# Performance work log

Measured on AMD Instinct MI355X. Metric: run time of the kernel, lower is better.

The kernel has to match this reference:

```python
import jax, jax.numpy as jnp
import numpy as np

NHEAD = 16
DHEAD = 128  # dim_embed // nhead
ROPE_BASE = 10000.0


def rmsnorm(x, g):
    eps = jnp.finfo(x.dtype).eps  # torch nn.RMSNorm default eps=None -> dtype eps
    return x * jax.lax.rsqrt(jnp.mean(x * x, axis=-1, keepdims=True) + eps) * g


def rope(x):
    # torchtune-style interleaved RoPE. x: [B,S,H,D]
    B, S, H, D = x.shape
    freqs = 1.0 / (ROPE_BASE ** (jnp.arange(0, D, 2, dtype=jnp.float32) / D))  # [D/2]
    ang = jnp.arange(S, dtype=jnp.float32)[:, None] * freqs[None, :]           # [S,D/2]
    cos = jnp.cos(ang)[None, :, None, :]
    sin = jnp.sin(ang)[None, :, None, :]
    x1, x2 = x[..., 0::2], x[..., 1::2]
    return jnp.stack([x1 * cos - x2 * sin, x1 * sin + x2 * cos], axis=-1).reshape(B, S, H, D)


def setup_inputs() -> dict:
    key = jax.random.key(0)
    B, S, E, C = 4, 2048, 2048, 512
    ks = jax.random.split(key, 9)
    std = 0.02
    h = jax.random.normal(ks[0], (B, S, E), jnp.float32)
    w_d_kv = jax.random.normal(ks[1], (C, E), jnp.float32) * std
    w_u_k = jax.random.normal(ks[2], (E, C), jnp.float32) * std
    w_u_v = jax.random.normal(ks[3], (E, C), jnp.float32) * std
    w_d_q = jax.random.normal(ks[4], (C, E), jnp.float32) * std
    w_u_q = jax.random.normal(ks[5], (E, C), jnp.float32) * std
    w_kr = jax.random.normal(ks[6], (E, E), jnp.float32) * std
    w_qr = jax.random.normal(ks[7], (E, C), jnp.float32) * std
    w_o = jax.random.normal(ks[8], (E, E), jnp.float32) * std
    g1 = jnp.ones((C,), jnp.float32)
    g2 = jnp.ones((C,), jnp.float32)
    g3 = jnp.ones((E,), jnp.float32)
    return {"h": h, "w_d_kv": w_d_kv, "w_u_k": w_u_k, "w_u_v": w_u_v,
            "w_d_q": w_d_q, "w_u_q": w_u_q, "w_kr": w_kr, "w_qr": w_qr,
            "w_o": w_o, "g1": g1, "g2": g2, "g3": g3}


def reference(h, w_d_kv, w_u_k, w_u_v, w_d_q, w_u_q, w_kr, w_qr, w_o, g1, g2, g3):
    # Eval (inference) path of MLA with absorbed weights; no kv/kr cache.
    B, S, E = h.shape
    cq = rmsnorm(h @ w_d_q.T, g1)          # [B,S,C]
    ckv = rmsnorm(h @ w_d_kv.T, g2)        # [B,S,C]
    qr = rope((cq @ w_qr.T).reshape(B, S, NHEAD, DHEAD)).reshape(B, S, E)
    kr = rope((h @ w_kr.T).reshape(B, S, NHEAD, DHEAD)).reshape(B, S, E)
    # absorbed_w_q = (w_d_q.T @ w_u_q.T) @ w_u_k : [E,C]
    absorbed_w_q = (w_d_q.T @ w_u_q.T) @ w_u_k
    # absorbed_w_o = w_u_v.T @ w_o.T : [C,E]
    absorbed_w_o = w_u_v.T @ w_o.T
    aq = h @ absorbed_w_q                  # [B,S,C]  (note: raw h, as in source)
    scores = jnp.einsum('bsc,btc->bst', aq, ckv) + jnp.einsum('bse,bte->bst', qr, kr)
    attn = jax.nn.softmax(scores / np.float32(np.sqrt(NHEAD + DHEAD)), axis=-1)
    o = jnp.einsum('bst,btc->bsc', attn, ckv)
    u = rmsnorm(o @ absorbed_w_o, g3)      # [B,S,E]
    return (u, ckv, kr)
```

## Files before the change

kernel.cpp:

```cpp
#include <hip/hip_runtime.h>
#include <stdint.h>

typedef __attribute__((ext_vector_type(8))) short bf16x8;
typedef __attribute__((ext_vector_type(8))) unsigned short u16x8;
typedef __attribute__((ext_vector_type(4))) float floatx4;

__device__ __forceinline__ uint16_t f2bf(float f) {
  union { float f; uint32_t u; } v; v.f = f;
  uint32_t r = v.u + 0x7fffu + ((v.u >> 16) & 1u);
  return (uint16_t)(r >> 16);
}
__device__ __forceinline__ float bf2f(uint16_t b) {
  union { uint32_t u; float f; } v; v.u = ((uint32_t)b) << 16;
  return v.f;
}
__device__ __forceinline__ float ld_as_float(float v) { return v; }
__device__ __forceinline__ float ld_as_float(uint16_t v) { return bf2f(v); }

__device__ __forceinline__ void mfma16(floatx4& d, bf16x8 a, bf16x8 b) {
  asm("v_mfma_f32_16x16x32_bf16 %0, %1, %2, %0" : "+v"(d) : "v"(a), "v"(b));
}

#define FENCE() asm volatile("" ::: "memory")
#define SCHED() __builtin_amdgcn_sched_barrier(0)
#define SBAR()                                  \
  do {                                          \
    FENCE();                                    \
    __builtin_amdgcn_sched_barrier(0);          \
    __builtin_amdgcn_s_barrier();               \
    __builtin_amdgcn_sched_barrier(0);          \
    FENCE();                                    \
  } while (0)

template<int MODE>
__global__ void __launch_bounds__(512, 1) gemm256v3(
    const uint16_t* __restrict__ A, const uint16_t* __restrict__ B,
    void* __restrict__ C0v, void* __restrict__ C1v, void* __restrict__ C2v,
    int K, int lda, int ldb, int ldc,
    long sA, long sB, long sC)
{
  __shared__ __attribute__((aligned(16))) char lds[131072];
  const int tid = threadIdx.x;
  const int w = tid >> 6, l = tid & 63;
  const int wm = w >> 2, wn = w & 3;

  const int gx = gridDim.x;
  const int nwg = gx * gridDim.y;
  int id = blockIdx.y * gx + blockIdx.x;
  if ((nwg & 7) == 0) id = (id & 7) * (nwg >> 3) + (id >> 3);
  const long bm = (long)(id % gx) * 256;
  const long bn = (long)(id / gx) * 256;
  A += (long)blockIdx.z * sA;
  B += (long)blockIdx.z * sB;

  const int scol = (((l & 3) ^ ((l >> 3) & 3)) << 3);
  const uint16_t* gA = A + (bm + w * 16 + (l >> 2)) * (long)lda + scol;
  const uint16_t* gB = B + (bn + w * 16 + (l >> 2)) * (long)ldb + scol;
  const int ldsw = w * 1024;

#define STG_A3(slot, k0, r)                                                    \
  __builtin_amdgcn_global_load_lds(gA + (k0) + (long)(r) * 128 * lda,          \
      (uint16_t*)(lds + (slot) * 32768 + (r) * 8192 + ldsw), 16, 0, 0)
#define STG_B3(slot, k0, r)                                                    \
  __builtin_amdgcn_global_load_lds(gB + (k0) + (long)(r) * 128 * ldb,          \
      (uint16_t*)(lds + (slot) * 32768 + 16384 + (r) * 8192 + ldsw), 16, 0, 0)

  const int lr = l & 15;
  const int chunkx = (((l >> 4) ^ ((lr >> 1) & 3)) << 4);
  const int aoff = (wm * 128 + lr) * 64 + chunkx;
  const int boff = 16384 + (wn * 64 + lr) * 64 + chunkx;

  floatx4 acc[8][4];
#pragma unroll
  for (int i = 0; i < 8; i++)
#pragma unroll
    for (int j = 0; j < 4; j++) acc[i][j] = (floatx4){0.f, 0.f, 0.f, 0.f};

  const int nt = K >> 5;
#pragma unroll
  for (int tt = 0; tt < 3; tt++) {
    STG_A3(tt, tt * 32, 0); STG_A3(tt, tt * 32, 1);
    STG_B3(tt, tt * 32, 0); STG_B3(tt, tt * 32, 1);
  }

  for (int t = 0; t < nt; t++) {
    const char* Ls = lds + (t & 3) * 32768;
    if (t + 2 < nt) asm volatile("s_waitcnt vmcnt(8)" ::: "memory");
    else            asm volatile("s_waitcnt vmcnt(0)" ::: "memory");
    SBAR();

    bf16x8 Bf[4], Af0[4], Af1[4];
#pragma unroll
    for (int j = 0; j < 4; j++) Bf[j] = *(const bf16x8*)(Ls + boff + j * 1024);
#pragma unroll
    for (int i = 0; i < 4; i++) Af0[i] = *(const bf16x8*)(Ls + aoff + i * 1024);
    SCHED();

    const long pk0 = (long)(t + 3) << 5;
    const int pslot = (t + 3) & 3;
    const bool pf = (t + 3 < nt);
    if (pf) { STG_A3(pslot, pk0, 0); STG_A3(pslot, pk0, 1); }

#pragma unroll
    for (int i = 0; i < 4; i++) Af1[i] = *(const bf16x8*)(Ls + aoff + (4 + i) * 1024);
    SCHED();

    asm volatile("s_waitcnt lgkmcnt(4)" ::: "memory");
    SCHED();
    __builtin_amdgcn_s_setprio(1);
#pragma unroll
    for (int i = 0; i < 4; i++)
#pragma unroll
      for (int j = 0; j < 4; j++) mfma16(acc[i][j], Af0[i], Bf[j]);
    __builtin_amdgcn_s_setprio(0);
    SCHED();

    if (pf) { STG_B3(pslot, pk0, 0); STG_B3(pslot, pk0, 1); }

    asm volatile("s_waitcnt lgkmcnt(0)" ::: "memory");
    SCHED();
    __builtin_amdgcn_s_setprio(1);
#pragma unroll
    for (int i = 0; i < 4; i++)
#pragma unroll
      for (int j = 0; j < 4; j++) mfma16(acc[4 + i][j], Af1[i], Bf[j]);
    __builtin_amdgcn_s_setprio(0);
    SCHED();
  }
#undef STG_A3
#undef STG_B3

  const long crow = bm + wm * 128 + ((l >> 4) * 4);
  const long ccol = bn + wn * 64 + (l & 15);
  if constexpr (MODE == 0) {
    float* C = (float*)C0v + (long)blockIdx.z * sC;
#pragma unroll
    for (int i = 0; i < 8; i++)
#pragma unroll
      for (int r = 0; r < 4; r++) {
        long row = crow + i * 16 + r;
#pragma unroll
        for (int j = 0; j < 4; j++) C[row * (long)ldc + ccol + j * 16] = acc[i][j][r];
      }
  } else if constexpr (MODE == 1) {
    uint16_t* C = (uint16_t*)C0v + (long)blockIdx.z * sC;
#pragma unroll
    for (int i = 0; i < 8; i++)
#pragma unroll
      for (int r = 0; r < 4; r++) {
        long row = crow + i * 16 + r;
#pragma unroll
        for (int j = 0; j < 4; j++) C[row * (long)ldc + ccol + j * 16] = f2bf(acc[i][j][r]);
      }
  } else if constexpr (MODE == 3) {
    const float s = 1.0f / 12.0f;
    uint16_t* C = (uint16_t*)C0v + (long)blockIdx.z * sC;
#pragma unroll
    for (int i = 0; i < 8; i++)
#pragma unroll
      for (int r = 0; r < 4; r++) {
        long row = crow + i * 16 + r;
#pragma unroll
        for (int j = 0; j < 4; j++) C[row * (long)ldc + ccol + j * 16] = f2bf(acc[i][j][r] * s);
      }
  } else {
    if (bn < 512) {
      uint16_t* C = (uint16_t*)C0v;
#pragma unroll
      for (int i = 0; i < 8; i++)
#pragma unroll
        for (int r = 0; r < 4; r++) {
          long row = crow + i * 16 + r;
#pragma unroll
          for (int j = 0; j < 4; j++) C[row * 512 + ccol + j * 16] = f2bf(acc[i][j][r]);
        }
    } else if (bn < 1024) {
      float* C = (float*)C1v;
      const long cc = ccol - 512;
#pragma unroll
      for (int i = 0; i < 8; i++)
#pragma unroll
        for (int r = 0; r < 4; r++) {
          long row = crow + i * 16 + r;
#pragma unroll
          for (int j = 0; j < 4; j++) C[row * 512 + cc + j * 16] = acc[i][j][r];
        }
    } else {
      uint16_t* C = (uint16_t*)C2v;
      const long cc = ccol - 1024;
#pragma unroll
      for (int i = 0; i < 8; i++)
#pragma unroll
        for (int r = 0; r < 4; r++) {
          long row = crow + i * 16 + r;
#pragma unroll
          for (int j = 0; j < 4; j++) C[row * 2560 + cc + j * 16] = f2bf(acc[i][j][r]);
        }
    }
  }
}

template<int OUTB>
__global__ void __launch_bounds__(512, 2) gemm256(
    const uint16_t* __restrict__ A, const uint16_t* __restrict__ B,
    void* __restrict__ Cv, int K, int lda, int ldb, int ldc,
    long sA, long sB, long sC)
{
  __shared__ __attribute__((aligned(16))) char lds[147456];
  const int tid = threadIdx.x;
  const int w = tid >> 6, l = tid & 63;
  const int wm = w >> 1, wn = w & 1;

  const int gx = gridDim.x;
  const int nwg = gx * gridDim.y;
  int id = blockIdx.y * gx + blockIdx.x;
  if ((nwg & 7) == 0) id = (id & 7) * (nwg >> 3) + (id >> 3);
  const long bm = (long)(id % gx) * 256;
  const long bn = (long)(id / gx) * 128;
  A += (long)blockIdx.z * sA;
  B += (long)blockIdx.z * sB;

  const int sr = l >> 3;
  const int sc = l & 7;
  const int scol = ((sc ^ sr) << 3);
  const uint16_t* gA = A + (bm + w * 8 + sr) * (long)lda + scol;
  const uint16_t* gB = B + (bn + w * 8 + sr) * (long)ldb + scol;
  const int ldsw = w * 1024;

#define STAGE_A(bufi, k0, r)                                                     \
  __builtin_amdgcn_global_load_lds(gA + (k0) + (long)(r) * 64 * lda,             \
      (uint16_t*)(lds + (bufi) * 49152 + (r) * 8192 + ldsw), 16, 0, 0)
#define STAGE_B(bufi, k0, r)                                                     \
  __builtin_amdgcn_global_load_lds(gB + (k0) + (long)(r) * 64 * ldb,             \
      (uint16_t*)(lds + (bufi) * 49152 + 32768 + (r) * 8192 + ldsw), 16, 0, 0)

  const int lr = l & 15;
  const int kk = (l >> 4) << 4;
  const int msk = (l & 7) << 4;
  const int ko0 = kk ^ msk;
  const int ko1 = (64 + kk) ^ msk;
  const int arow = (wm * 64 + lr) * 128;
  const int brow = (wn * 64 + lr) * 128;

  floatx4 acc[4][4];
#pragma unroll
  for (int i = 0; i < 4; i++)
#pragma unroll
    for (int j = 0; j < 4; j++) acc[i][j] = (floatx4){0.f, 0.f, 0.f, 0.f};

  const int nt = K >> 6;
#pragma unroll
  for (int r = 0; r < 4; r++) STAGE_A(0, 0, r);
#pragma unroll
  for (int r = 0; r < 2; r++) STAGE_B(0, 0, r);
#pragma unroll
  for (int r = 0; r < 4; r++) STAGE_A(1, 64, r);
#pragma unroll
  for (int r = 0; r < 2; r++) STAGE_B(1, 64, r);
  asm volatile("s_waitcnt vmcnt(6)" ::: "memory");
  SBAR();

  bf16x8 af0[4], bf0[4], af1[4], bf1[4];
  {
    const char* LA = lds + arow;
    const char* LB = lds + 32768 + brow;
#pragma unroll
    for (int i = 0; i < 4; i++) af0[i] = *(const bf16x8*)(LA + i * 2048 + ko0);
#pragma unroll
    for (int j = 0; j < 4; j++) bf0[j] = *(const bf16x8*)(LB + j * 2048 + ko0);
  }

  for (int t = 0; t < nt; t++) {
    const int buf = t % 3;
    const int pbuf = (t + 2) % 3;
    const long pk0 = (long)(t + 2) << 6;
    const char* LA = lds + buf * 49152 + arow;
    const char* LB = lds + buf * 49152 + 32768 + brow;
    const bool pf = (t + 2 < nt);

    if (pf) { STAGE_A(pbuf, pk0, 0); STAGE_A(pbuf, pk0, 1); STAGE_B(pbuf, pk0, 0); }
#pragma unroll
    for (int i = 0; i < 4; i++) af1[i] = *(const bf16x8*)(LA + i * 2048 + ko1);
#pragma unroll
    for (int j = 0; j < 4; j++) bf1[j] = *(const bf16x8*)(LB + j * 2048 + ko1);
    SCHED();
    __builtin_amdgcn_s_setprio(1);
#pragma unroll
    for (int i = 0; i < 4; i++)
#pragma unroll
      for (int j = 0; j < 4; j++) mfma16(acc[i][j], af0[i], bf0[j]);
    __builtin_amdgcn_s_setprio(0);
    SCHED();

    if (pf) { STAGE_A(pbuf, pk0, 2); STAGE_A(pbuf, pk0, 3); STAGE_B(pbuf, pk0, 1); }
    if (t < nt - 2) asm volatile("s_waitcnt vmcnt(6) lgkmcnt(0)" ::: "memory");
    else            asm volatile("s_waitcnt vmcnt(0) lgkmcnt(0)" ::: "memory");
    SBAR();
    if (t < nt - 1) {
      const char* LAn = lds + ((t + 1) % 3) * 49152 + arow;
      const char* LBn = lds + ((t + 1) % 3) * 49152 + 32768 + brow;
#pragma unroll
      for (int i = 0; i < 4; i++) af0[i] = *(const bf16x8*)(LAn + i * 2048 + ko0);
#pragma unroll
      for (int j = 0; j < 4; j++) bf0[j] = *(const bf16x8*)(LBn + j * 2048 + ko0);
    }
    SCHED();
    __builtin_amdgcn_s_setprio(1);
#pragma unroll
    for (int i = 0; i < 4; i++)
#pragma unroll
      for (int j = 0; j < 4; j++) mfma16(acc[i][j], af1[i], bf1[j]);
    __builtin_amdgcn_s_setprio(0);
    SCHED();
  }
#undef STAGE_A
#undef STAGE_B

  const long crow = bm + wm * 64 + ((l >> 4) * 4);
  const long ccol = bn + wn * 64 + (l & 15);
  if constexpr (OUTB == 0) {
    float* C = (float*)Cv + (long)blockIdx.z * sC;
#pragma unroll
    for (int i = 0; i < 4; i++)
#pragma unroll
      for (int r = 0; r < 4; r++) {
        long row = crow + i * 16 + r;
#pragma unroll
        for (int j = 0; j < 4; j++) C[row * (long)ldc + ccol + j * 16] = acc[i][j][r];
      }
  } else {
    uint16_t* C = (uint16_t*)Cv + (long)blockIdx.z * sC;
#pragma unroll
    for (int i = 0; i < 4; i++)
#pragma unroll
      for (int r = 0; r < 4; r++) {
        long row = crow + i * 16 + r;
#pragma unroll
        for (int j = 0; j < 4; j++) C[row * (long)ldc + ccol + j * 16] = f2bf(acc[i][j][r]);
      }
  }
}

template<int OUTB>
__global__ void __launch_bounds__(256) gemm_bt(
    const uint16_t* __restrict__ A, const uint16_t* __restrict__ B,
    void* __restrict__ Cv, int K, int lda, int ldb, int ldc,
    long sA, long sB, long sC)
{
  __shared__ alignas(16) uint16_t As[4096];
  __shared__ alignas(16) uint16_t Bs[4096];
  const int tid = threadIdx.x;
  const int w = tid >> 6, l = tid & 63;
  const int wr = w >> 1, wc = w & 1;
  const long bm = (long)blockIdx.x * 128, bn = (long)blockIdx.y * 128;
  A += (long)blockIdx.z * sA;
  B += (long)blockIdx.z * sB;

  const uint16_t* ga0 = A + (bm + w * 16 + (l >> 2)) * (long)lda + (l & 3) * 8;
  const uint16_t* ga1 = ga0 + 64L * lda;
  const uint16_t* gb0 = B + (bn + w * 16 + (l >> 2)) * (long)ldb + (l & 3) * 8;
  const uint16_t* gb1 = gb0 + 64L * ldb;
  uint16_t* la0 = &As[w * 512];
  uint16_t* la1 = &As[2048 + w * 512];
  uint16_t* lb0 = &Bs[w * 512];
  uint16_t* lb1 = &Bs[2048 + w * 512];

  floatx4 acc[4][4];
#pragma unroll
  for (int i = 0; i < 4; i++)
#pragma unroll
    for (int j = 0; j < 4; j++) acc[i][j] = (floatx4){0.f, 0.f, 0.f, 0.f};

  const int rA = (wr * 64 + (l & 15)) * 32 + (l >> 4) * 8;
  const int rB = (wc * 64 + (l & 15)) * 32 + (l >> 4) * 8;

  for (int k0 = 0; k0 < K; k0 += 32) {
    __builtin_amdgcn_global_load_lds(ga0, la0, 16, 0, 0);
    __builtin_amdgcn_global_load_lds(ga1, la1, 16, 0, 0);
    __builtin_amdgcn_global_load_lds(gb0, lb0, 16, 0, 0);
    __builtin_amdgcn_global_load_lds(gb1, lb1, 16, 0, 0);
    ga0 += 32; ga1 += 32; gb0 += 32; gb1 += 32;
    __syncthreads();
    bf16x8 af[4], bfr[4];
#pragma unroll
    for (int i = 0; i < 4; i++) af[i] = *(const bf16x8*)&As[rA + i * 512];
#pragma unroll
    for (int j = 0; j < 4; j++) bfr[j] = *(const bf16x8*)&Bs[rB + j * 512];
#pragma unroll
    for (int i = 0; i < 4; i++)
#pragma unroll
      for (int j = 0; j < 4; j++) mfma16(acc[i][j], af[i], bfr[j]);
    __syncthreads();
  }

  const long crow = bm + wr * 64 + ((l >> 4) * 4);
  const long ccol = bn + wc * 64 + (l & 15);
  if constexpr (OUTB == 0) {
    float* C = (float*)Cv + (long)blockIdx.z * sC;
#pragma unroll
    for (int i = 0; i < 4; i++)
#pragma unroll
      for (int r = 0; r < 4; r++) {
        long row = crow + i * 16 + r;
#pragma unroll
        for (int j = 0; j < 4; j++) C[row * (long)ldc + ccol + j * 16] = acc[i][j][r];
      }
  } else {
    uint16_t* C = (uint16_t*)Cv + (long)blockIdx.z * sC;
#pragma unroll
    for (int i = 0; i < 4; i++)
#pragma unroll
      for (int r = 0; r < 4; r++) {
        long row = crow + i * 16 + r;
#pragma unroll
        for (int j = 0; j < 4; j++) C[row * (long)ldc + ccol + j * 16] = f2bf(acc[i][j][r]);
      }
  }
}

__global__ void __launch_bounds__(256) cvt_k(const float* __restrict__ in,
                                             uint16_t* __restrict__ out, long n) {
  long i = ((long)blockIdx.x * 256 + threadIdx.x) * 4;
  if (i >= n) return;
  float4 v = *(const float4*)(in + i);
  ushort4 o; o.x = f2bf(v.x); o.y = f2bf(v.y); o.z = f2bf(v.z); o.w = f2bf(v.w);
  *(ushort4*)(out + i) = o;
}

__global__ void __launch_bounds__(256) prep_small(
    const float* __restrict__ wdq, const float* __restrict__ wdkv,
    const float* __restrict__ wqr, const float* __restrict__ wkr,
    const float* __restrict__ wo,
    uint16_t* __restrict__ wdq_b, uint16_t* __restrict__ wdkv_b,
    uint16_t* __restrict__ wqr_b, uint16_t* __restrict__ wkr_b,
    uint16_t* __restrict__ wo_b, float2* __restrict__ rtab)
{
  const int b = blockIdx.x;
  if (b < 11264) {
    const float* src; uint16_t* dst; long off;
    if (b < 1024)      { src = wdq;  dst = wdq_b;  off = b; }
    else if (b < 2048) { src = wdkv; dst = wdkv_b; off = b - 1024; }
    else if (b < 3072) { src = wqr;  dst = wqr_b;  off = b - 2048; }
    else if (b < 7168) { src = wkr;  dst = wkr_b;  off = b - 3072; }
    else               { src = wo;   dst = wo_b;   off = b - 7168; }
    long i = (off * 256 + threadIdx.x) * 4;
    float4 v = *(const float4*)(src + i);
    ushort4 o; o.x = f2bf(v.x); o.y = f2bf(v.y); o.z = f2bf(v.z); o.w = f2bf(v.w);
    *(ushort4*)(dst + i) = o;
  } else {
    int idx = (b - 11264) * 256 + threadIdx.x;
    int s = idx >> 6, fi = idx & 63;
    float f = powf(10000.0f, -(float)fi * (1.0f / 64.0f));
    float ang = (float)s * f;
    rtab[idx] = make_float2(cosf(ang), sinf(ang));
  }
}

template<typename TIN>
__global__ void __launch_bounds__(256) transpose_to_bf16(
    const TIN* __restrict__ in, uint16_t* __restrict__ out,
    int ld_in, int ld_out, long sIn, long sOut)
{
  __shared__ float tile[32][33];
  in += (long)blockIdx.z * sIn;
  out += (long)blockIdx.z * sOut;
  const int rb = blockIdx.y * 32, cb = blockIdx.x * 32;
#pragma unroll
  for (int i = 0; i < 32; i += 8)
    tile[threadIdx.y + i][threadIdx.x] =
        ld_as_float(in[(long)(rb + threadIdx.y + i) * ld_in + cb + threadIdx.x]);
  __syncthreads();
#pragma unroll
  for (int i = 0; i < 32; i += 8)
    out[(long)(cb + threadIdx.y + i) * ld_out + rb + threadIdx.x] =
        f2bf(tile[threadIdx.x][threadIdx.y + i]);
}

template<int PT, typename TIN>
__global__ void __launch_bounds__(256) rmsnorm_k(
    const TIN* __restrict__ in, const float* __restrict__ g,
    float* __restrict__ out_f, uint16_t* __restrict__ out_b, int ld_b)
{
  constexpr int DIM = PT * 256;
  __shared__ float sm[9];
  const TIN* x = in + (long)blockIdx.x * DIM;
  const int base = threadIdx.x * PT;
  float v[PT];
  if constexpr (sizeof(TIN) == 2) {
    if constexpr (PT >= 8) {
#pragma unroll
      for (int i = 0; i < PT; i += 8) {
        u16x8 t = *(const u16x8*)&x[base + i];
#pragma unroll
        for (int q = 0; q < 8; q++) v[i + q] = bf2f(t[q]);
      }
    } else {
#pragma unroll
      for (int i = 0; i < PT; i += 2) {
        ushort2 t = *(const ushort2*)&x[base + i];
        v[i] = bf2f(t.x); v[i + 1] = bf2f(t.y);
      }
    }
  } else if constexpr (PT == 2) {
    float2 t = *(const float2*)&x[base]; v[0] = t.x; v[1] = t.y;
  } else {
#pragma unroll
    for (int i = 0; i < PT; i += 4) {
      float4 t = *(const float4*)&x[base + i];
      v[i] = t.x; v[i + 1] = t.y; v[i + 2] = t.z; v[i + 3] = t.w;
    }
  }
  float ss = 0.f;
#pragma unroll
  for (int i = 0; i < PT; i++) ss += v[i] * v[i];
#pragma unroll
  for (int o = 32; o; o >>= 1) ss += __shfl_down(ss, o);
  if ((threadIdx.x & 63) == 0) sm[threadIdx.x >> 6] = ss;
  __syncthreads();
  if (threadIdx.x == 0)
    sm[8] = rsqrtf((sm[0] + sm[1] + sm[2] + sm[3]) * (1.0f / DIM) + 1.1920929e-7f);
  __syncthreads();
  const float sc = sm[8];
#pragma unroll
  for (int i = 0; i < PT; i++) {
    float y = v[i] * sc * g[base + i];
    if (out_f) out_f[(long)blockIdx.x * DIM + base + i] = y;
    if (out_b) out_b[(long)blockIdx.x * ld_b + base + i] = f2bf(y);
  }
}

template<bool WF32>
__global__ void __launch_bounds__(256) rope_k(
    const uint16_t* __restrict__ in, uint16_t* __restrict__ outb,
    float* __restrict__ outf, const float2* __restrict__ tab)
{
  long idx = (long)blockIdx.x * 256 + threadIdx.x;
  int r = (int)(idx >> 10);
  int pp = (int)idx & 1023;
  int s = r & 2047;
  int fi = pp & 63;
  ushort2 xv = *(const ushort2*)(in + ((long)r << 11) + 2 * pp);
  float x0 = bf2f(xv.x), x1 = bf2f(xv.y);
  float2 cs = tab[(s << 6) + fi];
  float y0 = x0 * cs.x - x1 * cs.y;
  float y1 = x0 * cs.y + x1 * cs.x;
  ushort2 ov; ov.x = f2bf(y0); ov.y = f2bf(y1);
  *(ushort2*)(outb + (long)r * 2560 + 512 + 2 * pp) = ov;
  if (WF32) *(float2*)(outf + ((long)r << 11) + 2 * pp) = make_float2(y0, y1);
}

__global__ void __launch_bounds__(256) softmax_k(const uint16_t* __restrict__ sc,
                                                 uint16_t* __restrict__ attn) {
  __shared__ float sm[9];
  const uint16_t* x = sc + ((long)blockIdx.x << 11);
  const int base = threadIdx.x * 8;
  float v[8];
  u16x8 t = *(const u16x8*)&x[base];
#pragma unroll
  for (int i = 0; i < 8; i++) v[i] = bf2f(t[i]);
  float m = -1e30f;
#pragma unroll
  for (int i = 0; i < 8; i++) m = fmaxf(m, v[i]);
#pragma unroll
  for (int o = 32; o; o >>= 1) m = fmaxf(m, __shfl_down(m, o));
  if ((threadIdx.x & 63) == 0) sm[threadIdx.x >> 6] = m;
  __syncthreads();
  if (threadIdx.x == 0)
    sm[8] = fmaxf(fmaxf(sm[0], sm[1]), fmaxf(sm[2], sm[3]));
  __syncthreads();
  m = sm[8];
  __syncthreads();
  float ss = 0.f;
#pragma unroll
  for (int i = 0; i < 8; i++) { v[i] = __expf(v[i] - m); ss += v[i]; }
#pragma unroll
  for (int o = 32; o; o >>= 1) ss += __shfl_down(ss, o);
  if ((threadIdx.x & 63) == 0) sm[threadIdx.x >> 6] = ss;
  __syncthreads();
  if (threadIdx.x == 0) sm[8] = 1.0f / (sm[0] + sm[1] + sm[2] + sm[3]);
  __syncthreads();
  const float r = sm[8];
  ushort4 o1, o2;
  o1.x = f2bf(v[0] * r); o1.y = f2bf(v[1] * r); o1.z = f2bf(v[2] * r); o1.w = f2bf(v[3] * r);
  o2.x = f2bf(v[4] * r); o2.y = f2bf(v[5] * r); o2.z = f2bf(v[6] * r); o2.w = f2bf(v[7] * r);
  uint16_t* dst = attn + ((long)blockIdx.x << 11) + base;
  *(ushort4*)dst = o1;
  *(ushort4*)(dst + 4) = o2;
}

extern "C" void kernel_launch(void* const* d_in, const int* in_sizes, int n_in,
                              void* d_out, int out_size, void* d_ws, size_t ws_size,
                              hipStream_t stream) {
  (void)in_sizes; (void)n_in; (void)out_size; (void)ws_size;
  const float* h    = (const float*)d_in[0];
  const float* wdkv = (const float*)d_in[1];
  const float* wuk  = (const float*)d_in[2];
  const float* wuv  = (const float*)d_in[3];
  const float* wdq  = (const float*)d_in[4];
  const float* wuq  = (const float*)d_in[5];
  const float* wkr  = (const float*)d_in[6];
  const float* wqr  = (const float*)d_in[7];
  const float* wo   = (const float*)d_in[8];
  const float* g1   = (const float*)d_in[9];
  const float* g2   = (const float*)d_in[10];
  const float* g3   = (const float*)d_in[11];

  float* u_out   = (float*)d_out;
  float* ckv_out = u_out + 16777216L;
  float* kr_out  = ckv_out + 4194304L;

  char* p = (char*)d_ws;
  auto alloc = [&](size_t bytes) -> void* {
    void* q = (void*)p; p += (bytes + 255) & ~(size_t)255; return q;
  };
  uint16_t* hb     = (uint16_t*)alloc(16777216ULL * 2);
  uint16_t* wcat   = (uint16_t*)alloc(3145728ULL * 2);
  uint16_t* wqr_b  = (uint16_t*)alloc(1048576ULL * 2);
  uint16_t* wkr_b  = (uint16_t*)alloc(4194304ULL * 2);
  uint16_t* wo_b   = (uint16_t*)alloc(4194304ULL * 2);
  uint16_t* wukT   = (uint16_t*)alloc(1048576ULL * 2);
  uint16_t* wuqT   = (uint16_t*)alloc(1048576ULL * 2);
  uint16_t* wuvT   = (uint16_t*)alloc(1048576ULL * 2);
  uint16_t* wdqT   = (uint16_t*)alloc(1048576ULL * 2);
  uint16_t* T1t    = (uint16_t*)alloc(262144ULL * 2);
  uint16_t* awoT   = (uint16_t*)alloc(1048576ULL * 2);
  uint16_t* cqpre  = (uint16_t*)alloc(4194304ULL * 2);
  uint16_t* cq_b   = (uint16_t*)alloc(4194304ULL * 2);
  uint16_t* catq   = (uint16_t*)alloc(20971520ULL * 2);
  uint16_t* catk   = (uint16_t*)alloc(20971520ULL * 2);
  uint16_t* ckvT   = (uint16_t*)alloc(4194304ULL * 2);
  uint16_t* o_b    = (uint16_t*)alloc(4194304ULL * 2);
  float2*   rtab   = (float2*)alloc(131072ULL * 8);
  float*    tmpS2  = (float*)alloc(4194304ULL * 4);
  float*    tmpB   = (float*)alloc(16777216ULL * 4);
  uint16_t* tmpBb  = (uint16_t*)tmpB;
  uint16_t* attn   = catq;

  uint16_t* wdq_b  = wcat;
  uint16_t* wdkv_b = wcat + 1048576;
  uint16_t* Bqt    = wcat + 2097152;

  const dim3 b256(256);
  const dim3 b512(512);
  const dim3 tb(32, 8);

  cvt_k<<<dim3(16384), b256, 0, stream>>>(h, hb, 16777216L);
  prep_small<<<dim3(11776), b256, 0, stream>>>(
      wdq, wdkv, wqr, wkr, wo, wdq_b, wdkv_b, wqr_b, wkr_b, wo_b, rtab);
  transpose_to_bf16<float><<<dim3(16, 64, 1), tb, 0, stream>>>(wuk, wukT, 512, 2048, 0, 0);
  transpose_to_bf16<float><<<dim3(16, 64, 1), tb, 0, stream>>>(wuq, wuqT, 512, 2048, 0, 0);
  transpose_to_bf16<float><<<dim3(16, 64, 1), tb, 0, stream>>>(wuv, wuvT, 512, 2048, 0, 0);
  transpose_to_bf16<float><<<dim3(64, 16, 1), tb, 0, stream>>>(wdq, wdqT, 2048, 512, 0, 0);

  gemm_bt<1><<<dim3(4, 4, 1), b256, 0, stream>>>(wukT, wuqT, T1t, 2048, 2048, 2048, 512, 0, 0, 0);
  gemm_bt<1><<<dim3(4, 16, 1), b256, 0, stream>>>(T1t, wdqT, Bqt, 512, 512, 512, 2048, 0, 0, 0);
  gemm_bt<1><<<dim3(16, 4, 1), b256, 0, stream>>>(wo_b, wuvT, awoT, 2048, 2048, 2048, 512, 0, 0, 0);

  gemm256v3<2><<<dim3(32, 6, 1), b512, 0, stream>>>(
      hb, wcat, cqpre, tmpS2, catq, 2048, 2048, 2048, 0, 0, 0, 0);
  rmsnorm_k<2, uint16_t><<<dim3(8192), b256, 0, stream>>>(cqpre, g1, nullptr, cq_b, 512);
  gemm256v3<1><<<dim3(32, 8, 1), b512, 0, stream>>>(
      cq_b, wqr_b, tmpBb, nullptr, nullptr, 512, 512, 512, 2048, 0, 0, 0);
  rope_k<false><<<dim3(32768), b256, 0, stream>>>(tmpBb, catq, nullptr, rtab);
  rmsnorm_k<2, float><<<dim3(8192), b256, 0, stream>>>(tmpS2, g2, ckv_out, catk, 2560);
  transpose_to_bf16<uint16_t><<<dim3(16, 64, 4), tb, 0, stream>>>(
      catk, ckvT, 2560, 2048, 2048L * 2560, 512L * 2048);
  gemm256v3<1><<<dim3(32, 8, 1), b512, 0, stream>>>(
      hb, wkr_b, tmpBb, nullptr, nullptr, 2048, 2048, 2048, 2048, 0, 0, 0);
  rope_k<true><<<dim3(32768), b256, 0, stream>>>(tmpBb, catk, kr_out, rtab);
  gemm256v3<3><<<dim3(8, 8, 4), b512, 0, stream>>>(
      catq, catk, tmpBb, nullptr, nullptr, 2560, 2560, 2560, 2048,
      5242880L, 5242880L, 4194304L);
  softmax_k<<<dim3(8192), b256, 0, stream>>>(tmpBb, attn);
  gemm256<1><<<dim3(8, 4, 4), b512, 0, stream>>>(
      attn, ckvT, o_b, 2048, 2048, 2048, 512, 4194304L, 1048576L, 1048576L);
  gemm256v3<1><<<dim3(32, 8, 1), b512, 0, stream>>>(
      o_b, awoT, tmpBb, nullptr, nullptr, 512, 512, 512, 2048, 0, 0, 0);
  rmsnorm_k<8, uint16_t><<<dim3(8192), b256, 0, stream>>>(tmpBb, g3, u_out, nullptr, 0);
}
```

Measured before the change: 551.5 us.

## Replace 256x256 GEMMs with 256x128 two-block-per-CU kernel and split-K weight absorption

Replaces the 512-thread 256x256 GEMM kernels with a 256-thread, 256x128-tile kernel. It uses a 3-slot LDS ring and launch bounds that allow two workgroups per CU, and it doubles grid sizes to match. The aim is better CU fill and latency hiding on the mid-sized projection and attention GEMMs. The K=2048 weight-absorption GEMMs are now split four ways along K, writing fp32 partials that a new reduceK kernel sums and converts to bf16. This exposes more parallelism for those small-output products, at the cost of extra launches and partial-buffer traffic.

```diff
diff --git a/kernel.cpp b/kernel.cpp
--- a/kernel.cpp
+++ b/kernel.cpp
@@ -33,180 +33,13 @@
   } while (0)
 
 template<int MODE>
-__global__ void __launch_bounds__(512, 1) gemm256v3(
+__global__ void __launch_bounds__(256, 2) gemm128(
     const uint16_t* __restrict__ A, const uint16_t* __restrict__ B,
     void* __restrict__ C0v, void* __restrict__ C1v, void* __restrict__ C2v,
     int K, int lda, int ldb, int ldc,
     long sA, long sB, long sC)
 {
-  __shared__ __attribute__((aligned(16))) char lds[131072];
-  const int tid = threadIdx.x;
-  const int w = tid >> 6, l = tid & 63;
-  const int wm = w >> 2, wn = w & 3;
-
-  const int gx = gridDim.x;
-  const int nwg = gx * gridDim.y;
-  int id = blockIdx.y * gx + blockIdx.x;
-  if ((nwg & 7) == 0) id = (id & 7) * (nwg >> 3) + (id >> 3);
-  const long bm = (long)(id % gx) * 256;
-  const long bn = (long)(id / gx) * 256;
-  A += (long)blockIdx.z * sA;
-  B += (long)blockIdx.z * sB;
-
-  const int scol = (((l & 3) ^ ((l >> 3) & 3)) << 3);
-  const uint16_t* gA = A + (bm + w * 16 + (l >> 2)) * (long)lda + scol;
-  const uint16_t* gB = B + (bn + w * 16 + (l >> 2)) * (long)ldb + scol;
-  const int ldsw = w * 1024;
-
-#define STG_A3(slot, k0, r)                                                    \
-  __builtin_amdgcn_global_load_lds(gA + (k0) + (long)(r) * 128 * lda,          \
-      (uint16_t*)(lds + (slot) * 32768 + (r) * 8192 + ldsw), 16, 0, 0)
-#define STG_B3(slot, k0, r)                                                    \
-  __builtin_amdgcn_global_load_lds(gB + (k0) + (long)(r) * 128 * ldb,          \
-      (uint16_t*)(lds + (slot) * 32768 + 16384 + (r) * 8192 + ldsw), 16, 0, 0)
-
-  const int lr = l & 15;
-  const int chunkx = (((l >> 4) ^ ((lr >> 1) & 3)) << 4);
-  const int aoff = (wm * 128 + lr) * 64 + chunkx;
-  const int boff = 16384 + (wn * 64 + lr) * 64 + chunkx;
-
-  floatx4 acc[8][4];
-#pragma unroll
-  for (int i = 0; i < 8; i++)
-#pragma unroll
-    for (int j = 0; j < 4; j++) acc[i][j] = (floatx4){0.f, 0.f, 0.f, 0.f};
-
-  const int nt = K >> 5;
-#pragma unroll
-  for (int tt = 0; tt < 3; tt++) {
-    STG_A3(tt, tt * 32, 0); STG_A3(tt, tt * 32, 1);
-    STG_B3(tt, tt * 32, 0); STG_B3(tt, tt * 32, 1);
-  }
-
-  for (int t = 0; t < nt; t++) {
-    const char* Ls = lds + (t & 3) * 32768;
-    if (t + 2 < nt) asm volatile("s_waitcnt vmcnt(8)" ::: "memory");
-    else            asm volatile("s_waitcnt vmcnt(0)" ::: "memory");
-    SBAR();
-
-    bf16x8 Bf[4], Af0[4], Af1[4];
-#pragma unroll
-    for (int j = 0; j < 4; j++) Bf[j] = *(const bf16x8*)(Ls + boff + j * 1024);
-#pragma unroll
-    for (int i = 0; i < 4; i++) Af0[i] = *(const bf16x8*)(Ls + aoff + i * 1024);
-    SCHED();
-
-    const long pk0 = (long)(t + 3) << 5;
-    const int pslot = (t + 3) & 3;
-    const bool pf = (t + 3 < nt);
-    if (pf) { STG_A3(pslot, pk0, 0); STG_A3(pslot, pk0, 1); }
-
-#pragma unroll
-    for (int i = 0; i < 4; i++) Af1[i] = *(const bf16x8*)(Ls + aoff + (4 + i) * 1024);
-    SCHED();
-
-    asm volatile("s_waitcnt lgkmcnt(4)" ::: "memory");
-    SCHED();
-    __builtin_amdgcn_s_setprio(1);
-#pragma unroll
-    for (int i = 0; i < 4; i++)
-#pragma unroll
-      for (int j = 0; j < 4; j++) mfma16(acc[i][j], Af0[i], Bf[j]);
-    __builtin_amdgcn_s_setprio(0);
-    SCHED();
-
-    if (pf) { STG_B3(pslot, pk0, 0); STG_B3(pslot, pk0, 1); }
-
-    asm volatile("s_waitcnt lgkmcnt(0)" ::: "memory");
-    SCHED();
-    __builtin_amdgcn_s_setprio(1);
-#pragma unroll
-    for (int i = 0; i < 4; i++)
-#pragma unroll
-      for (int j = 0; j < 4; j++) mfma16(acc[4 + i][j], Af1[i], Bf[j]);
-    __builtin_amdgcn_s_setprio(0);
-    SCHED();
-  }
-#undef STG_A3
-#undef STG_B3
-
-  const long crow = bm + wm * 128 + ((l >> 4) * 4);
-  const long ccol = bn + wn * 64 + (l & 15);
-  if constexpr (MODE == 0) {
-    float* C = (float*)C0v + (long)blockIdx.z * sC;
-#pragma unroll
-    for (int i = 0; i < 8; i++)
-#pragma unroll
-      for (int r = 0; r < 4; r++) {
-        long row = crow + i * 16 + r;
-#pragma unroll
-        for (int j = 0; j < 4; j++) C[row * (long)ldc + ccol + j * 16] = acc[i][j][r];
-      }
-  } else if constexpr (MODE == 1) {
-    uint16_t* C = (uint16_t*)C0v + (long)blockIdx.z * sC;
-#pragma unroll
-    for (int i = 0; i < 8; i++)
-#pragma unroll
-      for (int r = 0; r < 4; r++) {
-        long row = crow + i * 16 + r;
-#pragma unroll
-        for (int j = 0; j < 4; j++) C[row * (long)ldc + ccol + j * 16] = f2bf(acc[i][j][r]);
-      }
-  } else if constexpr (MODE == 3) {
-    const float s = 1.0f / 12.0f;
-    uint16_t* C = (uint16_t*)C0v + (long)blockIdx.z * sC;
-#pragma unroll
-    for (int i = 0; i < 8; i++)
-#pragma unroll
-      for (int r = 0; r < 4; r++) {
-        long row = crow + i * 16 + r;
-#pragma unroll
-        for (int j = 0; j < 4; j++) C[row * (long)ldc + ccol + j * 16] = f2bf(acc[i][j][r] * s);
-      }
-  } else {
-    if (bn < 512) {
-      uint16_t* C = (uint16_t*)C0v;
-#pragma unroll
-      for (int i = 0; i < 8; i++)
-#pragma unroll
-        for (int r = 0; r < 4; r++) {
-          long row = crow + i * 16 + r;
-#pragma unroll
-          for (int j = 0; j < 4; j++) C[row * 512 + ccol + j * 16] = f2bf(acc[i][j][r]);
-        }
-    } else if (bn < 1024) {
-      float* C = (float*)C1v;
-      const long cc = ccol - 512;
-#pragma unroll
-      for (int i = 0; i < 8; i++)
-#pragma unroll
-        for (int r = 0; r < 4; r++) {
-          long row = crow + i * 16 + r;
-#pragma unroll
-          for (int j = 0; j < 4; j++) C[row * 512 + cc + j * 16] = acc[i][j][r];
-        }
-    } else {
-      uint16_t* C = (uint16_t*)C2v;
-      const long cc = ccol - 1024;
-#pragma unroll
-      for (int i = 0; i < 8; i++)
-#pragma unroll
-        for (int r = 0; r < 4; r++) {
-          long row = crow + i * 16 + r;
-#pragma unroll
-          for (int j = 0; j < 4; j++) C[row * 2560 + cc + j * 16] = f2bf(acc[i][j][r]);
-        }
-    }
-  }
-}
-
-template<int OUTB>
-__global__ void __launch_bounds__(512, 2) gemm256(
-    const uint16_t* __restrict__ A, const uint16_t* __restrict__ B,
-    void* __restrict__ Cv, int K, int lda, int ldb, int ldc,
-    long sA, long sB, long sC)
-{
-  __shared__ __attribute__((aligned(16))) char lds[147456];
+  __shared__ __attribute__((aligned(16))) char lds[73728];
   const int tid = threadIdx.x;
   const int w = tid >> 6, l = tid & 63;
   const int wm = w >> 1, wn = w & 1;
@@ -220,124 +53,152 @@
   A += (long)blockIdx.z * sA;
   B += (long)blockIdx.z * sB;
 
-  const int sr = l >> 3;
-  const int sc = l & 7;
-  const int scol = ((sc ^ sr) << 3);
-  const uint16_t* gA = A + (bm + w * 8 + sr) * (long)lda + scol;
-  const uint16_t* gB = B + (bn + w * 8 + sr) * (long)ldb + scol;
+  const int scol = (((l & 3) ^ ((l >> 3) & 3)) << 3);
+  const uint16_t* gA = A + (bm + w * 16 + (l >> 2)) * (long)lda + scol;
+  const uint16_t* gB = B + (bn + w * 16 + (l >> 2)) * (long)ldb + scol;
   const int ldsw = w * 1024;
 
-#define STAGE_A(bufi, k0, r)                                                     \
-  __builtin_amdgcn_global_load_lds(gA + (k0) + (long)(r) * 64 * lda,             \
-      (uint16_t*)(lds + (bufi) * 49152 + (r) * 8192 + ldsw), 16, 0, 0)
-#define STAGE_B(bufi, k0, r)                                                     \
-  __builtin_amdgcn_global_load_lds(gB + (k0) + (long)(r) * 64 * ldb,             \
-      (uint16_t*)(lds + (bufi) * 49152 + 32768 + (r) * 8192 + ldsw), 16, 0, 0)
+#define STG_A4(slot, k0, r)                                                    \
+  __builtin_amdgcn_global_load_lds(gA + (k0) + (long)(r) * 64 * lda,           \
+      (uint16_t*)(lds + (slot) * 24576 + (r) * 4096 + ldsw), 16, 0, 0)
+#define STG_B4(slot, k0, r)                                                    \
+  __builtin_amdgcn_global_load_lds(gB + (k0) + (long)(r) * 64 * ldb,           \
+      (uint16_t*)(lds + (slot) * 24576 + 16384 + (r) * 4096 + ldsw), 16, 0, 0)
 
   const int lr = l & 15;
-  const int kk = (l >> 4) << 4;
-  const int msk = (l & 7) << 4;
-  const int ko0 = kk ^ msk;
-  const int ko1 = (64 + kk) ^ msk;
-  const int arow = (wm * 64 + lr) * 128;
-  const int brow = (wn * 64 + lr) * 128;
-
-  floatx4 acc[4][4];
-#pragma unroll
-  for (int i = 0; i < 4; i++)
+  const int chunkx = (((l >> 4) ^ ((lr >> 1) & 3)) << 4);
+  const int aoff = (wm * 128 + lr) * 64 + chunkx;
+  const int boff = 16384 + (wn * 64 + lr) * 64 + chunkx;
+
+  floatx4 acc[8][4];
+#pragma unroll
+  for (int i = 0; i < 8; i++)
 #pragma unroll
     for (int j = 0; j < 4; j++) acc[i][j] = (floatx4){0.f, 0.f, 0.f, 0.f};
 
-  const int nt = K >> 6;
-#pragma unroll
-  for (int r = 0; r < 4; r++) STAGE_A(0, 0, r);
-#pragma unroll
-  for (int r = 0; r < 2; r++) STAGE_B(0, 0, r);
-#pragma unroll
-  for (int r = 0; r < 4; r++) STAGE_A(1, 64, r);
-#pragma unroll
-  for (int r = 0; r < 2; r++) STAGE_B(1, 64, r);
-  asm volatile("s_waitcnt vmcnt(6)" ::: "memory");
-  SBAR();
-
-  bf16x8 af0[4], bf0[4], af1[4], bf1[4];
-  {
-    const char* LA = lds + arow;
-    const char* LB = lds + 32768 + brow;
-#pragma unroll
-    for (int i = 0; i < 4; i++) af0[i] = *(const bf16x8*)(LA + i * 2048 + ko0);
-#pragma unroll
-    for (int j = 0; j < 4; j++) bf0[j] = *(const bf16x8*)(LB + j * 2048 + ko0);
+  const int nt = K >> 5;
+#pragma unroll
+  for (int tt = 0; tt < 2; tt++) {
+    STG_A4(tt, tt * 32, 0); STG_A4(tt, tt * 32, 1);
+    STG_A4(tt, tt * 32, 2); STG_A4(tt, tt * 32, 3);
+    STG_B4(tt, tt * 32, 0); STG_B4(tt, tt * 32, 1);
   }
 
   for (int t = 0; t < nt; t++) {
-    const int buf = t % 3;
-    const int pbuf = (t + 2) % 3;
-    const long pk0 = (long)(t + 2) << 6;
-    const char* LA = lds + buf * 49152 + arow;
-    const char* LB = lds + buf * 49152 + 32768 + brow;
+    const char* Ls = lds + (t % 3) * 24576;
+    if (t < nt - 1) asm volatile("s_waitcnt vmcnt(6)" ::: "memory");
+    else            asm volatile("s_waitcnt vmcnt(0)" ::: "memory");
+    SBAR();
+
+    bf16x8 Bf[4], Af0[4], Af1[4];
+#pragma unroll
+    for (int j = 0; j < 4; j++) Bf[j] = *(const bf16x8*)(Ls + boff + j * 1024);
+#pragma unroll
+    for (int i = 0; i < 4; i++) Af0[i] = *(const bf16x8*)(Ls + aoff + i * 1024);
+    SCHED();
+
+    const long pk0 = (long)(t + 2) << 5;
+    const int pslot = (t + 2) % 3;
     const bool pf = (t + 2 < nt);
-
-    if (pf) { STAGE_A(pbuf, pk0, 0); STAGE_A(pbuf, pk0, 1); STAGE_B(pbuf, pk0, 0); }
-#pragma unroll
-    for (int i = 0; i < 4; i++) af1[i] = *(const bf16x8*)(LA + i * 2048 + ko1);
-#pragma unroll
-    for (int j = 0; j < 4; j++) bf1[j] = *(const bf16x8*)(LB + j * 2048 + ko1);
+    if (pf) { STG_A4(pslot, pk0, 0); STG_A4(pslot, pk0, 1); }
+
+#pragma unroll
+    for (int i = 0; i < 4; i++) Af1[i] = *(const bf16x8*)(Ls + aoff + (4 + i) * 1024);
+    SCHED();
+    if (pf) { STG_A4(pslot, pk0, 2); STG_A4(pslot, pk0, 3); }
+
+    asm volatile("s_waitcnt lgkmcnt(4)" ::: "memory");
     SCHED();
     __builtin_amdgcn_s_setprio(1);
 #pragma unroll
     for (int i = 0; i < 4; i++)
 #pragma unroll
-      for (int j = 0; j < 4; j++) mfma16(acc[i][j], af0[i], bf0[j]);
+      for (int j = 0; j < 4; j++) mfma16(acc[i][j], Af0[i], Bf[j]);
     __builtin_amdgcn_s_setprio(0);
     SCHED();
 
-    if (pf) { STAGE_A(pbuf, pk0, 2); STAGE_A(pbuf, pk0, 3); STAGE_B(pbuf, pk0, 1); }
-    if (t < nt - 2) asm volatile("s_waitcnt vmcnt(6) lgkmcnt(0)" ::: "memory");
-    else            asm volatile("s_waitcnt vmcnt(0) lgkmcnt(0)" ::: "memory");
-    SBAR();
-    if (t < nt - 1) {
-      const char* LAn = lds + ((t + 1) % 3) * 49152 + arow;
-      const char* LBn = lds + ((t + 1) % 3) * 49152 + 32768 + brow;
-#pragma unroll
-      for (int i = 0; i < 4; i++) af0[i] = *(const bf16x8*)(LAn + i * 2048 + ko0);
-#pragma unroll
-      for (int j = 0; j < 4; j++) bf0[j] = *(const bf16x8*)(LBn + j * 2048 + ko0);
-    }
+    if (pf) { STG_B4(pslot, pk0, 0); STG_B4(pslot, pk0, 1); }
+
+    asm volatile("s_waitcnt lgkmcnt(0)" ::: "memory");
     SCHED();
     __builtin_amdgcn_s_setprio(1);
 #pragma unroll
     for (int i = 0; i < 4; i++)
 #pragma unroll
-      for (int j = 0; j < 4; j++) mfma16(acc[i][j], af1[i], bf1[j]);
+      for (int j = 0; j < 4; j++) mfma16(acc[4 + i][j], Af1[i], Bf[j]);
     __builtin_amdgcn_s_setprio(0);
     SCHED();
   }
-#undef STAGE_A
-#undef STAGE_B
-
-  const long crow = bm + wm * 64 + ((l >> 4) * 4);
+#undef STG_A4
+#undef STG_B4
+
+  const long crow = bm + wm * 128 + ((l >> 4) * 4);
   const long ccol = bn + wn * 64 + (l & 15);
-  if constexpr (OUTB == 0) {
-    float* C = (float*)Cv + (long)blockIdx.z * sC;
-#pragma unroll
-    for (int i = 0; i < 4; i++)
+  if constexpr (MODE == 0) {
+    float* C = (float*)C0v + (long)blockIdx.z * sC;
+#pragma unroll
+    for (int i = 0; i < 8; i++)
 #pragma unroll
       for (int r = 0; r < 4; r++) {
         long row = crow + i * 16 + r;
 #pragma unroll
         for (int j = 0; j < 4; j++) C[row * (long)ldc + ccol + j * 16] = acc[i][j][r];
       }
-  } else {
-    uint16_t* C = (uint16_t*)Cv + (long)blockIdx.z * sC;
-#pragma unroll
-    for (int i = 0; i < 4; i++)
+  } else if constexpr (MODE == 1) {
+    uint16_t* C = (uint16_t*)C0v + (long)blockIdx.z * sC;
+#pragma unroll
+    for (int i = 0; i < 8; i++)
 #pragma unroll
       for (int r = 0; r < 4; r++) {
         long row = crow + i * 16 + r;
 #pragma unroll
         for (int j = 0; j < 4; j++) C[row * (long)ldc + ccol + j * 16] = f2bf(acc[i][j][r]);
       }
+  } else if constexpr (MODE == 3) {
+    const float s = 1.0f / 12.0f;
+    uint16_t* C = (uint16_t*)C0v + (long)blockIdx.z * sC;
+#pragma unroll
+    for (int i = 0; i < 8; i++)
+#pragma unroll
+      for (int r = 0; r < 4; r++) {
+        long row = crow + i * 16 + r;
+#pragma unroll
+        for (int j = 0; j < 4; j++) C[row * (long)ldc + ccol + j * 16] = f2bf(acc[i][j][r] * s);
+      }
+  } else {
+    if (bn < 512) {
+      uint16_t* C = (uint16_t*)C0v;
+#pragma unroll
+      for (int i = 0; i < 8; i++)
+#pragma unroll
+        for (int r = 0; r < 4; r++) {
+          long row = crow + i * 16 + r;
+#pragma unroll
+          for (int j = 0; j < 4; j++) C[row * 512 + ccol + j * 16] = f2bf(acc[i][j][r]);
+        }
+    } else if (bn < 1024) {
+      float* C = (float*)C1v;
+      const long cc = ccol - 512;
+#pragma unroll
+      for (int i = 0; i < 8; i++)
+#pragma unroll
+        for (int r = 0; r < 4; r++) {
+          long row = crow + i * 16 + r;
+#pragma unroll
+          for (int j = 0; j < 4; j++) C[row * 512 + cc + j * 16] = acc[i][j][r];
+        }
+    } else {
+      uint16_t* C = (uint16_t*)C2v;
+      const long cc = ccol - 1024;
+#pragma unroll
+      for (int i = 0; i < 8; i++)
+#pragma unroll
+        for (int r = 0; r < 4; r++) {
+          long row = crow + i * 16 + r;
+#pragma unroll
+          for (int j = 0; j < 4; j++) C[row * 2560 + cc + j * 16] = f2bf(acc[i][j][r]);
+        }
+    }
   }
 }
 
@@ -416,6 +277,20 @@
         for (int j = 0; j < 4; j++) C[row * (long)ldc + ccol + j * 16] = f2bf(acc[i][j][r]);
       }
   }
+}
+
+__global__ void __launch_bounds__(256) reduceK(const float* __restrict__ in,
+                                               uint16_t* __restrict__ out,
+                                               long n, int S, long stride) {
+  long i = ((long)blockIdx.x * 256 + threadIdx.x) * 4;
+  if (i >= n) return;
+  float4 s = *(const float4*)(in + i);
+  for (int k = 1; k < S; k++) {
+    float4 t = *(const float4*)(in + k * stride + i);
+    s.x += t.x; s.y += t.y; s.z += t.z; s.w += t.w;
+  }
+  ushort4 o; o.x = f2bf(s.x); o.y = f2bf(s.y); o.z = f2bf(s.z); o.w = f2bf(s.w);
+  *(ushort4*)(out + i) = o;
 }
 
 __global__ void __launch_bounds__(256) cvt_k(const float* __restrict__ in,
@@ -633,6 +508,8 @@
   float2*   rtab   = (float2*)alloc(131072ULL * 8);
   float*    tmpS2  = (float*)alloc(4194304ULL * 4);
   float*    tmpB   = (float*)alloc(16777216ULL * 4);
+  float*    redT   = (float*)alloc(1048576ULL * 4);
+  float*    redW   = (float*)alloc(4194304ULL * 4);
   uint16_t* tmpBb  = (uint16_t*)tmpB;
   uint16_t* attn   = catq;
 
@@ -641,7 +518,6 @@
   uint16_t* Bqt    = wcat + 2097152;
 
   const dim3 b256(256);
-  const dim3 b512(512);
   const dim3 tb(32, 8);
 
   cvt_k<<<dim3(16384), b256, 0, stream>>>(h, hb, 16777216L);
@@ -652,29 +528,34 @@
   transpose_to_bf16<float><<<dim3(16, 64, 1), tb, 0, stream>>>(wuv, wuvT, 512, 2048, 0, 0);
   transpose_to_bf16<float><<<dim3(64, 16, 1), tb, 0, stream>>>(wdq, wdqT, 2048, 512, 0, 0);
 
-  gemm_bt<1><<<dim3(4, 4, 1), b256, 0, stream>>>(wukT, wuqT, T1t, 2048, 2048, 2048, 512, 0, 0, 0);
+  gemm_bt<0><<<dim3(4, 4, 4), b256, 0, stream>>>(
+      wukT, wuqT, redT, 512, 2048, 2048, 512, 512L, 512L, 262144L);
+  reduceK<<<dim3(256), b256, 0, stream>>>(redT, T1t, 262144L, 4, 262144L);
+  gemm_bt<0><<<dim3(16, 4, 4), b256, 0, stream>>>(
+      wo_b, wuvT, redW, 512, 2048, 2048, 512, 512L, 512L, 1048576L);
+  reduceK<<<dim3(1024), b256, 0, stream>>>(redW, awoT, 1048576L, 4, 1048576L);
   gemm_bt<1><<<dim3(4, 16, 1), b256, 0, stream>>>(T1t, wdqT, Bqt, 512, 512, 512, 2048, 0, 0, 0);
-  gemm_bt<1><<<dim3(16, 4, 1), b256, 0, stream>>>(wo_b, wuvT, awoT, 2048, 2048, 2048, 512, 0, 0, 0);
-
-  gemm256v3<2><<<dim3(32, 6, 1), b512, 0, stream>>>(
+
+  gemm128<2><<<dim3(32, 12, 1), b256, 0, stream>>>(
       hb, wcat, cqpre, tmpS2, catq, 2048, 2048, 2048, 0, 0, 0, 0);
   rmsnorm_k<2, uint16_t><<<dim3(8192), b256, 0, stream>>>(cqpre, g1, nullptr, cq_b, 512);
-  gemm256v3<1><<<dim3(32, 8, 1), b512, 0, stream>>>(
+  gemm128<1><<<dim3(32, 16, 1), b256, 0, stream>>>(
       cq_b, wqr_b, tmpBb, nullptr, nullptr, 512, 512, 512, 2048, 0, 0, 0);
   rope_k<false><<<dim3(32768), b256, 0, stream>>>(tmpBb, catq, nullptr, rtab);
   rmsnorm_k<2, float><<<dim3(8192), b256, 0, stream>>>(tmpS2, g2, ckv_out, catk, 2560);
   transpose_to_bf16<uint16_t><<<dim3(16, 64, 4), tb, 0, stream>>>(
       catk, ckvT, 2560, 2048, 2048L * 2560, 512L * 2048);
-  gemm256v3<1><<<dim3(32, 8, 1), b512, 0, stream>>>(
+  gemm128<1><<<dim3(32, 16, 1), b256, 0, stream>>>(
       hb, wkr_b, tmpBb, nullptr, nullptr, 2048, 2048, 2048, 2048, 0, 0, 0);
   rope_k<true><<<dim3(32768), b256, 0, stream>>>(tmpBb, catk, kr_out, rtab);
-  gemm256v3<3><<<dim3(8, 8, 4), b512, 0, stream>>>(
+  gemm128<3><<<dim3(8, 16, 4), b256, 0, stream>>>(
       catq, catk, tmpBb, nullptr, nullptr, 2560, 2560, 2560, 2048,
       5242880L, 5242880L, 4194304L);
   softmax_k<<<dim3(8192), b256, 0, stream>>>(tmpBb, attn);
-  gemm256<1><<<dim3(8, 4, 4), b512, 0, stream>>>(
-      attn, ckvT, o_b, 2048, 2048, 2048, 512, 4194304L, 1048576L, 1048576L);
-  gemm256v3<1><<<dim3(32, 8, 1), b512, 0, stream>>>(
+  gemm128<1><<<dim3(8, 4, 4), b256, 0, stream>>>(
+      attn, ckvT, o_b, nullptr, nullptr, 2048, 2048, 2048, 512,
+      4194304L, 1048576L, 1048576L);
+  gemm128<1><<<dim3(32, 16, 1), b256, 0, stream>>>(
       o_b, awoT, tmpBb, nullptr, nullptr, 512, 512, 512, 2048, 0, 0, 0);
   rmsnorm_k<8, uint16_t><<<dim3(8192), b256, 0, stream>>>(tmpBb, g3, u_out, nullptr, 0);
 }
```

New measurement: 562.0 us. Within noise of the previous version (+1.9%).
